# Kernel tuning notes

Hardware: AMD Instinct MI355X
Metric: run time of the kernel (lower is better)

## Reference

```python
import jax, jax.numpy as jnp
import numpy as np

B, N, MAX_DIM = 8, 256, 2
D = 2 + MAX_DIM
EPS = 1e-8


def _lsa(cost):
    """Exact Jonker-Volgenant shortest-augmenting-path assignment (== scipy
    linear_sum_assignment) for a square cost matrix. Returns col4row."""
    n = cost.shape[0]
    u = np.zeros(n)
    v = np.zeros(n)
    col4row = np.full(n, -1)
    row4col = np.full(n, -1)
    for cur in range(n):
        shortest = np.full(n, np.inf)
        path = np.full(n, -1)
        SR = np.zeros(n, bool)
        SC = np.zeros(n, bool)
        i = cur
        minVal = 0.0
        sink = -1
        while sink == -1:
            SR[i] = True
            d = minVal + cost[i] - u[i] - v
            upd = (~SC) & (d < shortest)
            shortest[upd] = d[upd]
            path[upd] = i
            j = int(np.argmin(np.where(SC, np.inf, shortest)))
            minVal = shortest[j]
            SC[j] = True
            if row4col[j] == -1:
                sink = j
            else:
                i = row4col[j]
        u[cur] += minVal
        sr = SR.copy()
        sr[cur] = False
        ridx = np.where(sr)[0]
        u[ridx] += minVal - shortest[col4row[ridx]]
        cidx = np.where(SC)[0]
        v[cidx] -= minVal - shortest[cidx]
        j = sink
        while True:
            i = path[j]
            row4col[j] = i
            col4row[i], j = j, col4row[i]
            if i == cur:
                break
    return col4row


def _proj(p):
    # project point onto the diagonal midpoint: x' = x + sqrt(y+eps)/2, y' = 0
    return p[..., 0] + jnp.sqrt(p[..., 1] + EPS) / 2.0


def _dim_dist(set1, set2, dim):
    # NOTE: the torch code aliases set*_cur and set*_cur_projected, so the
    # in-place projection zeroes the y-coordinate of BOTH halves of each
    # concatenation. Hence every point is (proj_x, 0) and cdist(p=2)
    # degenerates to |x_a - x_b|. We reproduce that math faithfully.
    labels = jnp.argmax(set2[:, :, 2:], axis=2)                      # [B,N]
    s2 = (set2 * (labels == dim)[..., None])[:, :, :2]               # [B,N,2]
    s1 = (set1 * (set1[:, :, 2] == dim)[..., None])[:, :, :2]        # [B,N,2]
    p1 = _proj(s1)                                                   # [B,N]
    p2 = _proj(s2)                                                   # [B,N]
    a = jnp.concatenate([p1, p2], axis=0)                            # [2B,N]
    b = jnp.concatenate([p2, p1], axis=0)                            # [2B,N]
    return jnp.abs(a[:, :, None] - b[:, None, :])                    # [2B,N,N]


def _match(dist):
    dn = np.asarray(jax.lax.stop_gradient(dist))
    dn = np.where(np.isnan(dn), 1e6, dn)
    return jnp.asarray(np.stack([_lsa(c) for c in dn]))              # [2B,N]


def setup_inputs():
    key = jax.random.key(0)
    k1, k2, k3 = jax.random.split(key, 3)
    set1 = jax.random.uniform(k1, (B, N, D), dtype=jnp.float32)
    dims = jax.random.randint(k3, (B, N), 0, MAX_DIM).astype(jnp.float32)
    set1 = set1.at[:, :, 2].set(dims)  # integer homology-dim labels in col 2
    set2 = jax.random.uniform(k2, (B, N, D), dtype=jnp.float32)
    return {"set1": set1, "set2": set2}


def reference(set1, set2):
    max_dim = set2.shape[2] - 2
    total = jnp.float32(0.0)
    for dim in range(max_dim):
        dist = _dim_dist(set1, set2, dim)   # [2B,N,N]
        cols = _match(dist)                 # [2B,N] Hungarian assignment
        bb = jnp.arange(dist.shape[0])[:, None]
        rr = jnp.arange(dist.shape[1])[None, :]
        total = total + dist[bb, rr, cols].mean(axis=1).sum()
    return total
```

## Files before the change

### kernel.cpp

```cpp
#include <hip/hip_runtime.h>
#include <math.h>

#define PB 8
#define PN 256
#define PD 4
#define PEPS 1e-8f


__device__ __forceinline__ void cmpswap(float& lo, float& hi, bool up) {
    float mn = fminf(lo, hi);
    float mx = fmaxf(lo, hi);
    lo = up ? mn : mx;
    hi = up ? mx : mn;
}

__global__ __launch_bounds__(1024) void hung_kernel(
    const float* __restrict__ set1,
    const float* __restrict__ set2,
    float* __restrict__ out)
{
    const int tid  = threadIdx.x;
    const int wave = tid >> 6;
    const int lane = tid & 63;
    const int dim  = wave >> 3;
    const int b    = wave & 7;
    const float fdim = (float)dim;

    float p[4];
    float q[4];
    const float4* s1v = (const float4*)(set1 + (size_t)b * PN * PD);
    const float4* s2v = (const float4*)(set2 + (size_t)b * PN * PD);
    #pragma unroll
    for (int r = 0; r < 4; ++r) {
        int n = r * 64 + lane;
        float4 e1 = s1v[n];
        float4 e2 = s2v[n];
        bool m1 = (e1.z == fdim);
        int lab2 = (e2.w > e2.z) ? 1 : 0;
        bool m2 = (lab2 == dim);
        float mx1 = m1 ? e1.x : 0.0f, my1 = m1 ? e1.y : 0.0f;
        float mx2 = m2 ? e2.x : 0.0f, my2 = m2 ? e2.y : 0.0f;
        p[r] = mx1 + sqrtf(my1 + PEPS) * 0.5f;
        q[r] = mx2 + sqrtf(my2 + PEPS) * 0.5f;
    }

    #pragma unroll
    for (int k = 2; k <= 256; k <<= 1) {
        #pragma unroll
        for (int j = k >> 1; j > 0; j >>= 1) {
            if (j == 128) {
                cmpswap(p[0], p[2], true);  cmpswap(p[1], p[3], true);
                cmpswap(q[0], q[2], true);  cmpswap(q[1], q[3], true);
            } else if (j == 64) {
                bool up1 = (k == 256);
                cmpswap(p[0], p[1], true);  cmpswap(p[2], p[3], up1);
                cmpswap(q[0], q[1], true);  cmpswap(q[2], q[3], up1);
            } else {
                bool lower = ((lane & j) == 0);
                #pragma unroll
                for (int r = 0; r < 4; ++r) {
                    int idx = r * 64 + lane;
                    bool up = ((idx & k) == 0);
                    bool keepmin = (up == lower);
                    float po = __shfl_xor(p[r], j, 64);
                    float qo = __shfl_xor(q[r], j, 64);
                    float pmn = fminf(p[r], po), pmx = fmaxf(p[r], po);
                    float qmn = fminf(q[r], qo), qmx = fmaxf(q[r], qo);
                    p[r] = keepmin ? pmn : pmx;
                    q[r] = keepmin ? qmn : qmx;
                }
            }
        }
    }

    float v = 0.0f;
    #pragma unroll
    for (int r = 0; r < 4; ++r) v += fabsf(p[r] - q[r]);
    #pragma unroll
    for (int off = 32; off > 0; off >>= 1)
        v += __shfl_xor(v, off, 64);

    __shared__ float wsum[16];
    if (lane == 0) wsum[wave] = v;
    __syncthreads();
    if (tid == 0) {
        float s = 0.0f;
        #pragma unroll
        for (int i = 0; i < 16; ++i) s += wsum[i];
        out[0] = s * (2.0f / (float)PN);
    }
}

extern "C" void kernel_launch(void* const* d_in, const int* in_sizes, int n_in,
                              void* d_out, int out_size, void* d_ws, size_t ws_size,
                              hipStream_t stream) {
    const float* set1 = (const float*)d_in[0];
    const float* set2 = (const float*)d_in[1];
    float* out = (float*)d_out;

    hung_kernel<<<1, 1024, 0, stream>>>(set1, set2, out);
}
```

Before: 67.19 us.

## Split bitonic sort across 16 blocks with register-local passes and final reduction kernel

Each (dim, batch) wave now runs as its own single-wave block rather than sharing one 1024-thread block, and the per-block results are written to a workspace and summed by a second tiny kernel. Elements are laid out lane-major (four consecutive per lane), so the low-stride bitonic stages run inside registers and fewer cross-lane shuffles are needed. This spreads the work across CUs and cuts shuffle count, but adds a second kernel launch and a global round trip for the partial sums.

```diff
diff --git a/kernel.cpp b/kernel.cpp
--- a/kernel.cpp
+++ b/kernel.cpp
@@ -7,23 +7,42 @@
 #define PEPS 1e-8f
 
 
-__device__ __forceinline__ void cmpswap(float& lo, float& hi, bool up) {
-    float mn = fminf(lo, hi);
-    float mx = fmaxf(lo, hi);
-    lo = up ? mn : mx;
-    hi = up ? mx : mn;
+__device__ __forceinline__ void cswap(float& a, float& b, bool up) {
+    float mn = fminf(a, b);
+    float mx = fmaxf(a, b);
+    a = up ? mn : mx;
+    b = up ? mx : mn;
 }
 
-__global__ __launch_bounds__(1024) void hung_kernel(
+__device__ __forceinline__ void xpass(float (&p)[4], float (&q)[4],
+                                      int m, bool keepmin) {
+    #pragma unroll
+    for (int r = 0; r < 4; ++r) {
+        float po = __shfl_xor(p[r], m, 64);
+        float qo = __shfl_xor(q[r], m, 64);
+        float pmn = fminf(p[r], po), pmx = fmaxf(p[r], po);
+        float qmn = fminf(q[r], qo), qmx = fmaxf(q[r], qo);
+        p[r] = keepmin ? pmn : pmx;
+        q[r] = keepmin ? qmn : qmx;
+    }
+}
+
+__device__ __forceinline__ void lpass(float (&p)[4], float (&q)[4], bool up) {
+    cswap(p[0], p[2], up); cswap(p[1], p[3], up);
+    cswap(q[0], q[2], up); cswap(q[1], q[3], up);
+    cswap(p[0], p[1], up); cswap(p[2], p[3], up);
+    cswap(q[0], q[1], up); cswap(q[2], q[3], up);
+}
+
+__global__ __launch_bounds__(64) void hung_partial_kernel(
     const float* __restrict__ set1,
     const float* __restrict__ set2,
-    float* __restrict__ out)
+    float* __restrict__ partial)
 {
-    const int tid  = threadIdx.x;
-    const int wave = tid >> 6;
-    const int lane = tid & 63;
-    const int dim  = wave >> 3;
-    const int b    = wave & 7;
+    const int blk  = blockIdx.x;
+    const int dim  = blk >> 3;
+    const int b    = blk & 7;
+    const int lane = threadIdx.x;
     const float fdim = (float)dim;
 
     float p[4];
@@ -32,7 +51,7 @@
     const float4* s2v = (const float4*)(set2 + (size_t)b * PN * PD);
     #pragma unroll
     for (int r = 0; r < 4; ++r) {
-        int n = r * 64 + lane;
+        int n = lane * 4 + r;
         float4 e1 = s1v[n];
         float4 e2 = s2v[n];
         bool m1 = (e1.z == fdim);
@@ -44,49 +63,36 @@
         q[r] = mx2 + sqrtf(my2 + PEPS) * 0.5f;
     }
 
+    cswap(p[0], p[1], true);  cswap(p[2], p[3], false);
+    cswap(q[0], q[1], true);  cswap(q[2], q[3], false);
+    lpass(p, q, (lane & 1) == 0);
     #pragma unroll
-    for (int k = 2; k <= 256; k <<= 1) {
+    for (int k = 8; k <= 256; k <<= 1) {
+        bool up = (k == 256) ? true : ((lane & (k >> 2)) == 0);
         #pragma unroll
-        for (int j = k >> 1; j > 0; j >>= 1) {
-            if (j == 128) {
-                cmpswap(p[0], p[2], true);  cmpswap(p[1], p[3], true);
-                cmpswap(q[0], q[2], true);  cmpswap(q[1], q[3], true);
-            } else if (j == 64) {
-                bool up1 = (k == 256);
-                cmpswap(p[0], p[1], true);  cmpswap(p[2], p[3], up1);
-                cmpswap(q[0], q[1], true);  cmpswap(q[2], q[3], up1);
-            } else {
-                bool lower = ((lane & j) == 0);
-                #pragma unroll
-                for (int r = 0; r < 4; ++r) {
-                    int idx = r * 64 + lane;
-                    bool up = ((idx & k) == 0);
-                    bool keepmin = (up == lower);
-                    float po = __shfl_xor(p[r], j, 64);
-                    float qo = __shfl_xor(q[r], j, 64);
-                    float pmn = fminf(p[r], po), pmx = fmaxf(p[r], po);
-                    float qmn = fminf(q[r], qo), qmx = fmaxf(q[r], qo);
-                    p[r] = keepmin ? pmn : pmx;
-                    q[r] = keepmin ? qmn : qmx;
-                }
-            }
+        for (int m = k >> 3; m >= 1; m >>= 1) {
+            bool lower = ((lane & m) == 0);
+            xpass(p, q, m, up == lower);
         }
+        lpass(p, q, up);
     }
 
-    float v = 0.0f;
-    #pragma unroll
-    for (int r = 0; r < 4; ++r) v += fabsf(p[r] - q[r]);
+    float v = fabsf(p[0] - q[0]) + fabsf(p[1] - q[1])
+            + fabsf(p[2] - q[2]) + fabsf(p[3] - q[3]);
     #pragma unroll
     for (int off = 32; off > 0; off >>= 1)
         v += __shfl_xor(v, off, 64);
+    if (lane == 0) partial[blk] = v;
+}
 
-    __shared__ float wsum[16];
-    if (lane == 0) wsum[wave] = v;
-    __syncthreads();
-    if (tid == 0) {
+__global__ __launch_bounds__(64) void hung_final_kernel(
+    const float* __restrict__ partial,
+    float* __restrict__ out)
+{
+    if (threadIdx.x == 0) {
         float s = 0.0f;
         #pragma unroll
-        for (int i = 0; i < 16; ++i) s += wsum[i];
+        for (int i = 0; i < 16; ++i) s += partial[i];
         out[0] = s * (2.0f / (float)PN);
     }
 }
@@ -96,7 +102,9 @@
                               hipStream_t stream) {
     const float* set1 = (const float*)d_in[0];
     const float* set2 = (const float*)d_in[1];
+    float* partial = (float*)d_ws;
     float* out = (float*)d_out;
 
-    hung_kernel<<<1, 1024, 0, stream>>>(set1, set2, out);
+    hung_partial_kernel<<<16, 64, 0, stream>>>(set1, set2, partial);
+    hung_final_kernel<<<1, 64, 0, stream>>>(partial, out);
 }
```

After: 59.07 us. 12.1% less time.
